# Performance work log

Measured on AMD Instinct MI355X. Metric: run time of the kernel, lower is better.

The kernel has to match this reference:

```python
import jax, jax.numpy as jnp
import numpy as np

TAU = 1.0
EPS_MASS = 1e-6
EPS_LOG = 1e-8
EPS_DEN = 1e-8


def setup_inputs() -> dict:
    key = jax.random.key(0)
    k1, k2, k3, k4 = jax.random.split(key, 4)
    B, T, P, D, R, K = 4, 1024, 16, 64, 32, 64
    m = jax.random.normal(k1, (B, T, P, D), dtype=jnp.float32)
    w = jax.random.uniform(k2, (B, T, P), dtype=jnp.float32)
    p = jax.random.uniform(k3, (B, T, P, K), dtype=jnp.float32)
    patch_centers = jax.random.normal(k4, (R, D), dtype=jnp.float32)
    return {"m": m, "w": w, "p": p, "patch_centers": patch_centers}


def reference(m, w, p, patch_centers):
    # m: [B,T,P,D], w: [B,T,P], p: [B,T,P,K], patch_centers: [R,D]
    R = patch_centers.shape[0]
    # squared distances patch-component -> center: [B,T,P,R]
    diff = m[..., None, :] - patch_centers  # [B,T,P,R,D]
    dists = jnp.sum(diff * diff, axis=-1)
    gamma = jax.nn.softmax(-dists / TAU, axis=-1)  # [B,T,P,R]
    start_mass = gamma * w[..., None]  # [B,T,P,R]
    total_mass_r = start_mass.sum(axis=2)  # [B,T,R]
    p_bar_num = jnp.einsum('btpk,btpr->btrk', p, start_mass)  # [B,T,R,K]
    p_bar = p_bar_num / (total_mass_r[..., None] + EPS_MASS)
    # pairwise center affinity omega: [R,R]
    cdiff = patch_centers[:, None, :] - patch_centers[None, :, :]
    center_dists = jnp.sum(cdiff * cdiff, axis=-1)
    omega = jnp.exp(-center_dists / TAU)
    # pairwise JS divergence over K: [B,T,R,R]
    p_r = p_bar[:, :, :, None, :]  # [B,T,R,1,K]
    p_s = p_bar[:, :, None, :, :]  # [B,T,1,R,K]
    m_dist = 0.5 * (p_r + p_s)
    log_m = jnp.log(m_dist + EPS_LOG)
    kl_r = jnp.sum(p_r * (jnp.log(p_r + EPS_LOG) - log_m), axis=-1)
    kl_s = jnp.sum(p_s * (jnp.log(p_s + EPS_LOG) - log_m), axis=-1)
    js_rs = 0.5 * (kl_r + kl_s)  # [B,T,R,R]
    weighted_js = omega * js_rs
    mask = jnp.triu(jnp.ones((R, R), dtype=jnp.float32), k=1)
    loss = jnp.sum(weighted_js * mask) / (jnp.sum(mask) + EPS_DEN)
    return loss
```

## Files before the change

kernel.cpp:

```cpp
#include <hip/hip_runtime.h>

#define PP 16
#define DD 64
#define RR 32
#define KK 64
#define NBT 4096

#define LOG2E 1.4426950408889634f
#define LN2   0.6931471805599453f
#define D2_CUT 25.0f

static __device__ __forceinline__ float fast_log2(float x) { return __builtin_amdgcn_logf(x); }
static __device__ __forceinline__ float fast_exp2(float x) { return __builtin_amdgcn_exp2f(x); }
static __device__ __forceinline__ float fast_rcp(float x)  { return __builtin_amdgcn_rcpf(x); }

__global__ __launch_bounds__(1024) void prune_kernel(const float* __restrict__ c,
                                                     float* __restrict__ cc,
                                                     int* __restrict__ meta,
                                                     float2* __restrict__ plist) {
    __shared__ float red[16];
    __shared__ float dmin_sh;
    __shared__ int cnt;
    const int t = threadIdx.x;
    const int r = t >> 5, s = t & 31;
    const bool active = s > r;
    const float4* c4 = (const float4*)c;

    float d2 = 0.f;
#pragma unroll
    for (int d4 = 0; d4 < 16; ++d4) {
        float4 a = c4[r * 16 + d4];
        float4 b = c4[s * 16 + d4];
        float dx = a.x - b.x, dy = a.y - b.y, dz = a.z - b.z, dw = a.w - b.w;
        d2 = fmaf(dx, dx, d2); d2 = fmaf(dy, dy, d2);
        d2 = fmaf(dz, dz, d2); d2 = fmaf(dw, dw, d2);
    }
    if (t == 0) cnt = 0;
    float dm = active ? d2 : 3.4e38f;
#pragma unroll
    for (int off = 32; off > 0; off >>= 1) dm = fminf(dm, __shfl_down(dm, off, 64));
    if ((t & 63) == 0) red[t >> 6] = dm;
    __syncthreads();
    if (t < 64) {
        float v = (t < 16) ? red[t] : 3.4e38f;
#pragma unroll
        for (int off = 8; off > 0; off >>= 1) v = fminf(v, __shfl_down(v, off, 64));
        if (t == 0) dmin_sh = v;
    }
    __syncthreads();
    if (active && d2 <= dmin_sh + D2_CUT) {
        int idx = atomicAdd(&cnt, 1);
        plist[idx] = make_float2(fast_exp2(-d2 * LOG2E), __int_as_float(t));
    }
    if (t < RR) {
        float a2 = 0.f;
#pragma unroll
        for (int d4 = 0; d4 < 16; ++d4) {
            float4 v = c4[t * 16 + d4];
            a2 = fmaf(v.x, v.x, a2); a2 = fmaf(v.y, v.y, a2);
            a2 = fmaf(v.z, v.z, a2); a2 = fmaf(v.w, v.w, a2);
        }
        cc[t] = a2;
    }
    __syncthreads();
    if (t == 0) meta[0] = cnt;
}

__global__ __launch_bounds__(256) void sheaf2_kernel(
    const float* __restrict__ m, const float* __restrict__ w,
    const float* __restrict__ p, const float* __restrict__ c,
    const float* __restrict__ cc, const int* __restrict__ meta,
    const float2* __restrict__ plist, float* __restrict__ partials) {
    __shared__ __align__(16) float  sm_m[PP * DD];
    __shared__ __align__(16) float  sm_p[PP * KK];
    __shared__ __align__(16) float2 smem_cpl[RR * KK];
    __shared__ __align__(16) float  sm_mass[PP * 36];
    __shared__ float sm_w[PP];
    __shared__ float sred[4];

    float2* sm_cT2 = smem_cpl;
    float2* sm_pl  = smem_cpl;

    const int tid = threadIdx.x;
    const int bt  = blockIdx.x;
    const int k   = tid & 63;
    const int wv  = tid >> 6;
    const int r   = tid & 31;
    const int pg  = tid >> 5;
    const int np  = meta[0];

    {
        const float4* m4 = (const float4*)(m + (size_t)bt * PP * DD);
        const float4* p4 = (const float4*)(p + (size_t)bt * PP * KK);
        ((float4*)sm_m)[tid] = m4[tid];
        ((float4*)sm_p)[tid] = p4[tid];
        const float2* c2 = (const float2*)c;
#pragma unroll
        for (int it = 0; it < 4; ++it) {
            int idx = tid + 256 * it;
            sm_cT2[(idx & 31) * 33 + (idx >> 5)] = c2[idx];
        }
        if (tid < PP) sm_w[tid] = w[(size_t)bt * PP + tid];
    }
    __syncthreads();

    {
        float ccr = cc[r];
        float acc0 = 0.f, acc1 = 0.f;
#pragma unroll
        for (int d4 = 0; d4 < 16; ++d4) {
            float2 ca = sm_cT2[(2 * d4) * 33 + r];
            float2 cb = sm_cT2[(2 * d4 + 1) * 33 + r];
            float4 ma = *(const float4*)&sm_m[pg * DD + d4 * 4];
            float4 mb = *(const float4*)&sm_m[(pg + 8) * DD + d4 * 4];
            acc0 = fmaf(ma.x, ca.x, acc0); acc0 = fmaf(ma.y, ca.y, acc0);
            acc0 = fmaf(ma.z, cb.x, acc0); acc0 = fmaf(ma.w, cb.y, acc0);
            acc1 = fmaf(mb.x, ca.x, acc1); acc1 = fmaf(mb.y, ca.y, acc1);
            acc1 = fmaf(mb.z, cb.x, acc1); acc1 = fmaf(mb.w, cb.y, acc1);
        }
        float l0 = fmaf(2.f, acc0, -ccr);
        float l1 = fmaf(2.f, acc1, -ccr);
        float mx0 = l0, mx1 = l1;
#pragma unroll
        for (int off = 1; off <= 16; off <<= 1) {
            mx0 = fmaxf(mx0, __shfl_xor(mx0, off, 64));
            mx1 = fmaxf(mx1, __shfl_xor(mx1, off, 64));
        }
        float e0 = fast_exp2((l0 - mx0) * LOG2E);
        float e1 = fast_exp2((l1 - mx1) * LOG2E);
        float s0 = e0, s1 = e1;
#pragma unroll
        for (int off = 1; off <= 16; off <<= 1) {
            s0 += __shfl_xor(s0, off, 64);
            s1 += __shfl_xor(s1, off, 64);
        }
        float sw0 = sm_w[pg]     * fast_rcp(s0);
        float sw1 = sm_w[pg + 8] * fast_rcp(s1);
        sm_mass[pg * 36 + r]       = e0 * sw0;
        sm_mass[(pg + 8) * 36 + r] = e1 * sw1;
    }
    __syncthreads();

    float inv;
    {
        float tot = 0.f;
#pragma unroll
        for (int pi = 0; pi < PP; ++pi) tot += sm_mass[pi * 36 + r];
        inv = fast_rcp(tot + 1e-6f);
    }

    {
        const int r0 = wv * 8;
        float acc[8] = {0.f, 0.f, 0.f, 0.f, 0.f, 0.f, 0.f, 0.f};
#pragma unroll
        for (int pi = 0; pi < PP; ++pi) {
            float pv = sm_p[pi * KK + k];
            float4 ma = *(const float4*)&sm_mass[pi * 36 + r0];
            float4 mb = *(const float4*)&sm_mass[pi * 36 + r0 + 4];
            acc[0] = fmaf(pv, ma.x, acc[0]);
            acc[1] = fmaf(pv, ma.y, acc[1]);
            acc[2] = fmaf(pv, ma.z, acc[2]);
            acc[3] = fmaf(pv, ma.w, acc[3]);
            acc[4] = fmaf(pv, mb.x, acc[4]);
            acc[5] = fmaf(pv, mb.y, acc[5]);
            acc[6] = fmaf(pv, mb.z, acc[6]);
            acc[7] = fmaf(pv, mb.w, acc[7]);
        }
#pragma unroll
        for (int j = 0; j < 8; ++j) {
            float pb = acc[j] * __shfl(inv, r0 + j, 64);
            float l2 = fast_log2(pb + 1e-8f);
            sm_pl[(r0 + j) * KK + k] = make_float2(pb, pb * l2);
        }
    }
    __syncthreads();

    {
        float acc = 0.f;
        for (int i = wv; i < np; i += 4) {
            float2 e = plist[i];
            int rs = __float_as_int(e.y);
            int rr = rs >> 5, ss = rs & 31;
            float2 a = sm_pl[rr * KK + k];
            float2 b = sm_pl[ss * KK + k];
            float sum = a.x + b.x;
            float t   = a.y + b.y;
            float lm  = fast_log2(fmaf(0.5f, sum, 1e-8f));
            t = fmaf(-sum, lm, t);
            acc = fmaf(e.x, t, acc);
        }
#pragma unroll
        for (int off = 32; off > 0; off >>= 1) acc += __shfl_down(acc, off, 64);
        if (k == 0) sred[wv] = acc;
    }
    __syncthreads();
    if (tid == 0) {
        float tot = (sred[0] + sred[1]) + (sred[2] + sred[3]);
        partials[bt] = tot * (0.5f * LN2 / 496.0f);
    }
}

__global__ __launch_bounds__(256) void reduce_kernel(const float* __restrict__ partials,
                                                     float* __restrict__ out) {
    __shared__ float sred[4];
    const int tid = threadIdx.x;
    const float4* p4 = (const float4*)partials;
    float acc = 0.f;
#pragma unroll
    for (int i = 0; i < 4; ++i) {
        float4 v = p4[tid + 256 * i];
        acc += (v.x + v.y) + (v.z + v.w);
    }
#pragma unroll
    for (int off = 32; off > 0; off >>= 1) acc += __shfl_down(acc, off, 64);
    if ((tid & 63) == 0) sred[tid >> 6] = acc;
    __syncthreads();
    if (tid == 0) out[0] = (sred[0] + sred[1]) + (sred[2] + sred[3]);
}

extern "C" void kernel_launch(void* const* d_in, const int* in_sizes, int n_in,
                              void* d_out, int out_size, void* d_ws, size_t ws_size,
                              hipStream_t stream) {
    const float* m = (const float*)d_in[0];
    const float* w = (const float*)d_in[1];
    const float* p = (const float*)d_in[2];
    const float* c = (const float*)d_in[3];
    float* out = (float*)d_out;

    float* wsf      = (float*)d_ws;
    int*   meta     = (int*)d_ws;
    float* cc       = wsf + 64;
    float2* plist   = (float2*)(wsf + 128);
    float* partials = wsf + 2048;

    prune_kernel<<<1, 1024, 0, stream>>>(c, cc, meta, plist);
    sheaf2_kernel<<<NBT, 256, 0, stream>>>(m, w, p, c, cc, meta, plist, partials);
    reduce_kernel<<<1, 256, 0, stream>>>(partials, out);
}
```

Baseline: 114.0 us.

## Read m, p and prepacked centers directly from global, drop shared staging

Centers are prepacked once in the prune kernel into a d4-major float4 layout. The main kernel then reads m, p and the centers straight from global/L2 instead of staging them in shared memory, and accumulates per-center mass totals with LDS atomics. It also splits the pbar computation differently across threads and stores pbar and pbar*log in transposed, padded shared arrays. The aim is to cut LDS footprint and staging traffic to raise occupancy, at the cost of more global and cache loads plus atomics.

```diff
diff --git a/kernel.cpp b/kernel.cpp
--- a/kernel.cpp
+++ b/kernel.cpp
@@ -17,7 +17,8 @@
 __global__ __launch_bounds__(1024) void prune_kernel(const float* __restrict__ c,
                                                      float* __restrict__ cc,
                                                      int* __restrict__ meta,
-                                                     float2* __restrict__ plist) {
+                                                     float2* __restrict__ plist,
+                                                     float4* __restrict__ c_packed) {
     __shared__ float red[16];
     __shared__ float dmin_sh;
     __shared__ int cnt;
@@ -26,6 +27,8 @@
     const bool active = s > r;
     const float4* c4 = (const float4*)c;
 
+    if (t < 512) c_packed[t] = c4[(t & 31) * 16 + (t >> 5)];
+
     float d2 = 0.f;
 #pragma unroll
     for (int d4 = 0; d4 < 16; ++d4) {
@@ -66,58 +69,43 @@
     if (t == 0) meta[0] = cnt;
 }
 
-__global__ __launch_bounds__(256) void sheaf2_kernel(
+__global__ __launch_bounds__(256, 4) void sheaf3_kernel(
     const float* __restrict__ m, const float* __restrict__ w,
-    const float* __restrict__ p, const float* __restrict__ c,
-    const float* __restrict__ cc, const int* __restrict__ meta,
-    const float2* __restrict__ plist, float* __restrict__ partials) {
-    __shared__ __align__(16) float  sm_m[PP * DD];
-    __shared__ __align__(16) float  sm_p[PP * KK];
-    __shared__ __align__(16) float2 smem_cpl[RR * KK];
-    __shared__ __align__(16) float  sm_mass[PP * 36];
-    __shared__ float sm_w[PP];
+    const float* __restrict__ p, const float* __restrict__ cc,
+    const int* __restrict__ meta, const float2* __restrict__ plist,
+    const float4* __restrict__ c_packed, float* __restrict__ partials) {
+    __shared__ float sm_mass[PP * 36];
+    __shared__ float sm_tot[RR];
+    __shared__ float sm_pbT[KK * 33];
+    __shared__ float sm_plT[KK * 33];
     __shared__ float sred[4];
 
-    float2* sm_cT2 = smem_cpl;
-    float2* sm_pl  = smem_cpl;
-
-    const int tid = threadIdx.x;
-    const int bt  = blockIdx.x;
-    const int k   = tid & 63;
-    const int wv  = tid >> 6;
-    const int r   = tid & 31;
-    const int pg  = tid >> 5;
-    const int np  = meta[0];
+    const int tid  = threadIdx.x;
+    const int bt   = blockIdx.x;
+    const int lane = tid & 63;
+    const int wv   = tid >> 6;
+    const int np   = meta[0];
+
+    if (tid < RR) sm_tot[tid] = 0.f;
+    __syncthreads();
 
     {
-        const float4* m4 = (const float4*)(m + (size_t)bt * PP * DD);
-        const float4* p4 = (const float4*)(p + (size_t)bt * PP * KK);
-        ((float4*)sm_m)[tid] = m4[tid];
-        ((float4*)sm_p)[tid] = p4[tid];
-        const float2* c2 = (const float2*)c;
-#pragma unroll
-        for (int it = 0; it < 4; ++it) {
-            int idx = tid + 256 * it;
-            sm_cT2[(idx & 31) * 33 + (idx >> 5)] = c2[idx];
-        }
-        if (tid < PP) sm_w[tid] = w[(size_t)bt * PP + tid];
-    }
-    __syncthreads();
-
-    {
+        const int r  = tid & 31;
+        const int pg = tid >> 5;
+        const float4* m4a = (const float4*)(m + (size_t)bt * PP * DD) + pg * 16;
+        const float4* m4b = m4a + 8 * 16;
+        float acc0 = 0.f, acc1 = 0.f;
+#pragma unroll
+        for (int d4 = 0; d4 < 16; ++d4) {
+            float4 cv = c_packed[d4 * 32 + r];
+            float4 ma = m4a[d4];
+            float4 mb = m4b[d4];
+            acc0 = fmaf(ma.x, cv.x, acc0); acc0 = fmaf(ma.y, cv.y, acc0);
+            acc0 = fmaf(ma.z, cv.z, acc0); acc0 = fmaf(ma.w, cv.w, acc0);
+            acc1 = fmaf(mb.x, cv.x, acc1); acc1 = fmaf(mb.y, cv.y, acc1);
+            acc1 = fmaf(mb.z, cv.z, acc1); acc1 = fmaf(mb.w, cv.w, acc1);
+        }
         float ccr = cc[r];
-        float acc0 = 0.f, acc1 = 0.f;
-#pragma unroll
-        for (int d4 = 0; d4 < 16; ++d4) {
-            float2 ca = sm_cT2[(2 * d4) * 33 + r];
-            float2 cb = sm_cT2[(2 * d4 + 1) * 33 + r];
-            float4 ma = *(const float4*)&sm_m[pg * DD + d4 * 4];
-            float4 mb = *(const float4*)&sm_m[(pg + 8) * DD + d4 * 4];
-            acc0 = fmaf(ma.x, ca.x, acc0); acc0 = fmaf(ma.y, ca.y, acc0);
-            acc0 = fmaf(ma.z, cb.x, acc0); acc0 = fmaf(ma.w, cb.y, acc0);
-            acc1 = fmaf(mb.x, ca.x, acc1); acc1 = fmaf(mb.y, ca.y, acc1);
-            acc1 = fmaf(mb.z, cb.x, acc1); acc1 = fmaf(mb.w, cb.y, acc1);
-        }
         float l0 = fmaf(2.f, acc0, -ccr);
         float l1 = fmaf(2.f, acc1, -ccr);
         float mx0 = l0, mx1 = l1;
@@ -134,57 +122,66 @@
             s0 += __shfl_xor(s0, off, 64);
             s1 += __shfl_xor(s1, off, 64);
         }
-        float sw0 = sm_w[pg]     * fast_rcp(s0);
-        float sw1 = sm_w[pg + 8] * fast_rcp(s1);
-        sm_mass[pg * 36 + r]       = e0 * sw0;
-        sm_mass[(pg + 8) * 36 + r] = e1 * sw1;
-    }
-    __syncthreads();
-
-    float inv;
+        float w0 = w[(size_t)bt * PP + pg];
+        float w1 = w[(size_t)bt * PP + pg + 8];
+        float v0 = e0 * (w0 * fast_rcp(s0));
+        float v1 = e1 * (w1 * fast_rcp(s1));
+        sm_mass[pg * 36 + r]       = v0;
+        sm_mass[(pg + 8) * 36 + r] = v1;
+        float tp = v0 + v1;
+        tp += __shfl_xor(tp, 32, 64);
+        if (lane < 32) atomicAdd(&sm_tot[r], tp);
+    }
+    __syncthreads();
+
     {
-        float tot = 0.f;
-#pragma unroll
-        for (int pi = 0; pi < PP; ++pi) tot += sm_mass[pi * 36 + r];
-        inv = fast_rcp(tot + 1e-6f);
-    }
+        const int rp = lane & 15;
+        const int kb = lane >> 4;
+        const int r0 = rp * 2;
+        const int k0 = wv * 16 + kb * 4;
+        const float4* p4 = (const float4*)(p + (size_t)bt * PP * KK);
+        float2 t2 = *(const float2*)&sm_tot[r0];
+        float inv0 = fast_rcp(t2.x + 1e-6f);
+        float inv1 = fast_rcp(t2.y + 1e-6f);
+        float a0[4] = {0.f, 0.f, 0.f, 0.f};
+        float a1[4] = {0.f, 0.f, 0.f, 0.f};
+#pragma unroll
+        for (int pi = 0; pi < PP; ++pi) {
+            float2 mv = *(const float2*)&sm_mass[pi * 36 + r0];
+            float4 pv = p4[pi * 16 + (k0 >> 2)];
+            a0[0] = fmaf(mv.x, pv.x, a0[0]); a0[1] = fmaf(mv.x, pv.y, a0[1]);
+            a0[2] = fmaf(mv.x, pv.z, a0[2]); a0[3] = fmaf(mv.x, pv.w, a0[3]);
+            a1[0] = fmaf(mv.y, pv.x, a1[0]); a1[1] = fmaf(mv.y, pv.y, a1[1]);
+            a1[2] = fmaf(mv.y, pv.z, a1[2]); a1[3] = fmaf(mv.y, pv.w, a1[3]);
+        }
+#pragma unroll
+        for (int kk = 0; kk < 4; ++kk) {
+            int ko = (k0 + kk) * 33;
+            float pb0 = a0[kk] * inv0;
+            float pb1 = a1[kk] * inv1;
+            float lg0 = fast_log2(pb0 + 1e-8f);
+            float lg1 = fast_log2(pb1 + 1e-8f);
+            sm_pbT[ko + r0]     = pb0;
+            sm_pbT[ko + r0 + 1] = pb1;
+            sm_plT[ko + r0]     = pb0 * lg0;
+            sm_plT[ko + r0 + 1] = pb1 * lg1;
+        }
+    }
+    __syncthreads();
 
     {
-        const int r0 = wv * 8;
-        float acc[8] = {0.f, 0.f, 0.f, 0.f, 0.f, 0.f, 0.f, 0.f};
-#pragma unroll
-        for (int pi = 0; pi < PP; ++pi) {
-            float pv = sm_p[pi * KK + k];
-            float4 ma = *(const float4*)&sm_mass[pi * 36 + r0];
-            float4 mb = *(const float4*)&sm_mass[pi * 36 + r0 + 4];
-            acc[0] = fmaf(pv, ma.x, acc[0]);
-            acc[1] = fmaf(pv, ma.y, acc[1]);
-            acc[2] = fmaf(pv, ma.z, acc[2]);
-            acc[3] = fmaf(pv, ma.w, acc[3]);
-            acc[4] = fmaf(pv, mb.x, acc[4]);
-            acc[5] = fmaf(pv, mb.y, acc[5]);
-            acc[6] = fmaf(pv, mb.z, acc[6]);
-            acc[7] = fmaf(pv, mb.w, acc[7]);
-        }
-#pragma unroll
-        for (int j = 0; j < 8; ++j) {
-            float pb = acc[j] * __shfl(inv, r0 + j, 64);
-            float l2 = fast_log2(pb + 1e-8f);
-            sm_pl[(r0 + j) * KK + k] = make_float2(pb, pb * l2);
-        }
-    }
-    __syncthreads();
-
-    {
+        const int k = lane;
         float acc = 0.f;
         for (int i = wv; i < np; i += 4) {
             float2 e = plist[i];
             int rs = __float_as_int(e.y);
             int rr = rs >> 5, ss = rs & 31;
-            float2 a = sm_pl[rr * KK + k];
-            float2 b = sm_pl[ss * KK + k];
-            float sum = a.x + b.x;
-            float t   = a.y + b.y;
+            float par = sm_pbT[k * 33 + rr];
+            float pas = sm_pbT[k * 33 + ss];
+            float lar = sm_plT[k * 33 + rr];
+            float las = sm_plT[k * 33 + ss];
+            float sum = par + pas;
+            float t   = lar + las;
             float lm  = fast_log2(fmaf(0.5f, sum, 1e-8f));
             t = fmaf(-sum, lm, t);
             acc = fmaf(e.x, t, acc);
@@ -227,13 +224,14 @@
     const float* c = (const float*)d_in[3];
     float* out = (float*)d_out;
 
-    float* wsf      = (float*)d_ws;
-    int*   meta     = (int*)d_ws;
-    float* cc       = wsf + 64;
-    float2* plist   = (float2*)(wsf + 128);
-    float* partials = wsf + 2048;
-
-    prune_kernel<<<1, 1024, 0, stream>>>(c, cc, meta, plist);
-    sheaf2_kernel<<<NBT, 256, 0, stream>>>(m, w, p, c, cc, meta, plist, partials);
+    float* wsf       = (float*)d_ws;
+    int*    meta     = (int*)d_ws;
+    float*  cc       = wsf + 64;
+    float2* plist    = (float2*)(wsf + 128);
+    float4* c_packed = (float4*)(wsf + 2048);
+    float*  partials = wsf + 4096;
+
+    prune_kernel<<<1, 1024, 0, stream>>>(c, cc, meta, plist, c_packed);
+    sheaf3_kernel<<<NBT, 256, 0, stream>>>(m, w, p, cc, meta, plist, c_packed, partials);
     reduce_kernel<<<1, 256, 0, stream>>>(partials, out);
 }
```

After: 122.9 us. 1.08x slower.
